# Performance work log

Hardware: AMD Instinct MI355X
Metric: run time of the kernel (lower is better)

## Reference

```python
import jax, jax.numpy as jnp
import numpy as np

NUM_LAYERS = 6
D = 16           # physical_dim == bond_dim (required for multi-layer consistency)
B, S, FIN = 128, 2048, 128


def setup_inputs() -> dict:
    key = jax.random.key(0)
    k0, k1, k2, k3 = jax.random.split(key, 4)
    return {
        "sequence": jax.random.normal(k0, (B, S, FIN), jnp.float32),
        "W_emb": jax.random.normal(k1, (FIN, D), jnp.float32) * 0.05,
        "b_emb": jnp.zeros((D,), jnp.float32),
        "u": jax.random.normal(k2, (NUM_LAYERS, D, D, D, D), jnp.float32) * 0.1,
        "w": jax.random.normal(k3, (NUM_LAYERS, D, D, D), jnp.float32) * 0.1,
    }


def _ent_entropy(sA, sB):
    # sA: (B, pA, d), sB: (B, pB, d)
    corr = jnp.einsum('bik,bjk->bij', sA, sB)          # (B, pA, pB)
    s = jnp.linalg.svd(corr, compute_uv=False)          # (B, min(pA,pB))
    sn = s / (jnp.sum(s, axis=1, keepdims=True) + 1e-8)
    return -jnp.sum(sn * jnp.log(sn + 1e-8), axis=1)    # (B,)


def _phi_q(sites):
    # sites: (B, n, d), n >= 4 and even
    n = sites.shape[1]
    mid = n // 2
    S_int = _ent_entropy(sites[:, :mid], sites[:, mid:])
    A, Bp = sites[:, :mid], sites[:, mid:]
    S1 = _ent_entropy(A[:, :mid // 2], A[:, mid // 2:])
    S2 = _ent_entropy(Bp[:, :(n - mid) // 2], Bp[:, (n - mid) // 2:])
    return jnp.maximum(S_int - (S1 + S2), 0.0)


def _apply_layer(sites, u_l, w_l):
    # sites: (B, n, d) with n even. Disentangle adjacent pairs, then coarse-grain.
    b, n, d = sites.shape
    s = sites.reshape(b, n // 2, 2, d)
    # disentangler: einsum('ijkl,bi,bj->bkl') batched over pairs p
    comb = jnp.einsum('ijkl,bpi,bpj->bpkl', u_l, s[:, :, 0], s[:, :, 1])
    o1 = comb.mean(axis=3)   # mean over l -> (b, p, k)
    o2 = comb.mean(axis=2)   # mean over k -> (b, p, l)
    # isometry acts on consecutive disentangled pairs (o1_i, o2_i)
    return jnp.einsum('aij,bpi,bpj->bpa', w_l, o1, o2)  # (b, n//2, bond)


def reference(sequence, W_emb, b_emb, u, w):
    emb = sequence @ W_emb + b_emb                       # (B, S, D)
    norm = jnp.linalg.norm(emb, axis=-1, keepdims=True)
    sites = emb / jnp.maximum(norm, 1e-12)               # F.normalize(dim=-1)
    for l in range(NUM_LAYERS):
        sites = _apply_layer(sites, u[l], w[l])
    phi_q = _phi_q(sites)
    return sites, phi_q
```

## Files before the change

### kernel.cpp

```cpp
#include <hip/hip_runtime.h>
#include <hip/hip_bf16.h>
#include <math.h>

#define BATCH 128
#define SEQ   2048
#define FIN   128
#define DD    16
#define NLAYERS 6
#define SST   20
#define SWEEPS 8

#define BUFA_F  (BATCH*SEQ*DD)
#define BUFB_F  (BATCH*(SEQ/2)*DD)
#define COEF_OFF (BUFA_F + BUFB_F)
#define ENT_OFF  (COEF_OFF + NLAYERS*12288)

__global__ __launch_bounds__(256) void k_front(const float* __restrict__ seq,
                                               const float* __restrict__ W,
                                               const float* __restrict__ bias,
                                               const float* __restrict__ u,
                                               const float* __restrict__ w,
                                               float* __restrict__ coef,
                                               float* __restrict__ out) {
    __shared__ float sW[2048];
    __shared__ float sR[64*132];
    int t = threadIdx.x;
    if (blockIdx.x < 6) {
        int l  = blockIdx.x;
        int ij = t;
        const float* ub = u + (size_t)l*65536 + (size_t)ij*256;
        float a1[16], a2[16];
#pragma unroll
        for (int k = 0; k < 16; ++k) { a1[k] = 0.0f; a2[k] = 0.0f; }
#pragma unroll
        for (int k = 0; k < 16; ++k) {
#pragma unroll
            for (int z = 0; z < 16; ++z) {
                float v = ub[k*16 + z];
                a1[k] += v;
                a2[z] += v;
            }
        }
        float* ucb = coef + (size_t)l*12288 + ij*32;
#pragma unroll
        for (int k = 0; k < 16; ++k) {
            ucb[k]      = a1[k]*(1.0f/16.0f);
            ucb[16 + k] = a2[k]*(1.0f/16.0f);
        }
        const float* wb = w + (size_t)l*4096;
        float* wtb = coef + (size_t)l*12288 + 8192 + ij*16;
#pragma unroll
        for (int a = 0; a < 16; ++a) wtb[a] = wb[a*256 + ij];
        return;
    }
    size_t rowbase = (size_t)(blockIdx.x - 6) * 64;
    for (int x = t; x < 2048; x += 256) sW[x] = W[x];
    {
        const float4* seq4 = (const float4*)seq + rowbase*32;
#pragma unroll
        for (int it = 0; it < 8; ++it) {
            int idx = t + it*256;
            int r = idx >> 5, kk = idx & 31;
            *(float4*)&sR[r*132 + kk*4] = seq4[idx];
        }
    }
    int q = t & 3, lr = t >> 2;
    float acc[4];
    {
        float4 bv = *(const float4*)(bias + q*4);
        acc[0] = bv.x; acc[1] = bv.y; acc[2] = bv.z; acc[3] = bv.w;
    }
    __syncthreads();

#pragma unroll 8
    for (int kk = 0; kk < 32; ++kk) {
        float4 rv = *(const float4*)&sR[lr*132 + kk*4];
        float rc[4] = { rv.x, rv.y, rv.z, rv.w };
#pragma unroll
        for (int c = 0; c < 4; ++c) {
            float4 wv = *(const float4*)&sW[(kk*4 + c)*16 + q*4];
            float s = rc[c];
            acc[0] = fmaf(s, wv.x, acc[0]);
            acc[1] = fmaf(s, wv.y, acc[1]);
            acc[2] = fmaf(s, wv.z, acc[2]);
            acc[3] = fmaf(s, wv.w, acc[3]);
        }
    }
    float p = 0.0f;
#pragma unroll
    for (int j = 0; j < 4; ++j) p = fmaf(acc[j], acc[j], p);
    p += __shfl_xor(p, 1);
    p += __shfl_xor(p, 2);
    float inv = 1.0f / fmaxf(sqrtf(p), 1e-12f);
    *(float4*)(out + (rowbase + lr)*16 + q*4) = make_float4(acc[0]*inv, acc[1]*inv,
                                                            acc[2]*inv, acc[3]*inv);
}

__global__ __launch_bounds__(256) void k_layer(const float* __restrict__ in,
                                               float* __restrict__ outp,
                                               const float* __restrict__ coefl) {
    __shared__ float cbuf[8192];
    __shared__ float spl[64*36];
    int t = threadIdx.x;
    int og = t & 7, pg = t >> 3;
    int lane = t & 63, base = lane & ~7;

    const float4* wtf = (const float4*)(coefl + 8192);
    float4 wr0 = wtf[0*256 + t];
    float4 wr1 = wtf[1*256 + t];
    float4 wr2 = wtf[2*256 + t];
    float4 wr3 = wtf[3*256 + t];

    {
        const float4* ucf = (const float4*)coefl;
        float4* c4 = (float4*)cbuf;
#pragma unroll
        for (int it = 0; it < 8; ++it) c4[it*256 + t] = ucf[it*256 + t];
    }
    {
        const float4* ing = (const float4*)in + (size_t)blockIdx.x*512;
        float4 v0 = ing[t];
        float4 v1 = ing[t + 256];
        *(float4*)&spl[(t >> 3)*36 + (t & 7)*4]        = v0;
        *(float4*)&spl[((t >> 3) + 32)*36 + (t & 7)*4] = v1;
    }
    __syncthreads();

    float s1v[2][16];
#pragma unroll
    for (int pp = 0; pp < 2; ++pp) {
        int p = pg + pp*32;
#pragma unroll
        for (int g = 0; g < 4; ++g) {
            float4 v = *(const float4*)&spl[p*36 + 16 + g*4];
            s1v[pp][g*4+0]=v.x; s1v[pp][g*4+1]=v.y; s1v[pp][g*4+2]=v.z; s1v[pp][g*4+3]=v.w;
        }
    }

    float accv[2][4];
    accv[0][0]=0.f; accv[0][1]=0.f; accv[0][2]=0.f; accv[0][3]=0.f;
    accv[1][0]=0.f; accv[1][1]=0.f; accv[1][2]=0.f; accv[1][3]=0.f;

    for (int i = 0; i < 16; ++i) {
        float s0a = spl[pg*36 + i];
        float s0b = spl[(pg + 32)*36 + i];
        const float4* uc = (const float4*)&cbuf[i*512] + og;
#pragma unroll
        for (int j = 0; j < 16; ++j) {
            float4 cv = uc[j*8];
            float pa = s0a * s1v[0][j];
            float pb = s0b * s1v[1][j];
            accv[0][0] = fmaf(pa, cv.x, accv[0][0]);
            accv[0][1] = fmaf(pa, cv.y, accv[0][1]);
            accv[0][2] = fmaf(pa, cv.z, accv[0][2]);
            accv[0][3] = fmaf(pa, cv.w, accv[0][3]);
            accv[1][0] = fmaf(pb, cv.x, accv[1][0]);
            accv[1][1] = fmaf(pb, cv.y, accv[1][1]);
            accv[1][2] = fmaf(pb, cv.z, accv[1][2]);
            accv[1][3] = fmaf(pb, cv.w, accv[1][3]);
        }
    }
    __syncthreads();
    {
        float4* c4 = (float4*)cbuf;
        c4[0*256 + t] = wr0;
        c4[1*256 + t] = wr1;
        c4[2*256 + t] = wr2;
        c4[3*256 + t] = wr3;
    }
    __syncthreads();

    float o2f[2][16];
#pragma unroll
    for (int j = 0; j < 16; ++j) {
        int src = base + 4 + (j >> 2);
        o2f[0][j] = __shfl(accv[0][j & 3], src, 64);
        o2f[1][j] = __shfl(accv[1][j & 3], src, 64);
    }

    float r0a = 0.f, r1a = 0.f, r0b = 0.f, r1b = 0.f;
    for (int grp = 0; grp < 4; ++grp) {
#pragma unroll
        for (int c = 0; c < 4; ++c) {
            float o1a = __shfl(accv[0][c], base + grp, 64);
            float o1b = __shfl(accv[1][c], base + grp, 64);
            const float2* wrow = (const float2*)&cbuf[(grp*4 + c)*256] + og;
#pragma unroll
            for (int j = 0; j < 16; ++j) {
                float2 wv = wrow[j*8];
                float qa = o1a * o2f[0][j];
                float qb = o1b * o2f[1][j];
                r0a = fmaf(qa, wv.x, r0a);
                r1a = fmaf(qa, wv.y, r1a);
                r0b = fmaf(qb, wv.x, r0b);
                r1b = fmaf(qb, wv.y, r1b);
            }
        }
    }

    size_t gp = (size_t)blockIdx.x*64;
    *(float2*)&outp[(gp + pg)*16 + og*2]      = make_float2(r0a, r1a);
    *(float2*)&outp[(gp + pg + 32)*16 + og*2] = make_float2(r0b, r1b);
}

template<int P, bool LAST>
__device__ __forceinline__ void layer_body(float* sL, const float* coef,
                                           float* outp, int npg, int t, int bid) {
    int og = t & 7, pg = t >> 3;
    int lane = t & 63, base = lane & ~7;
    bool act = pg < npg;

    float accv[P][4];
    float s1v[P][16];
#pragma unroll
    for (int pp = 0; pp < P; ++pp) { accv[pp][0]=0.f; accv[pp][1]=0.f; accv[pp][2]=0.f; accv[pp][3]=0.f; }

    if (act) {
#pragma unroll
        for (int pp = 0; pp < P; ++pp) {
            int r = 2*(pg + pp*32) + 1;
#pragma unroll
            for (int g = 0; g < 4; ++g) {
                float4 v = *(const float4*)&sL[r*SST + g*4];
                s1v[pp][g*4+0]=v.x; s1v[pp][g*4+1]=v.y; s1v[pp][g*4+2]=v.z; s1v[pp][g*4+3]=v.w;
            }
        }
        for (int i = 0; i < 16; ++i) {
            float s0[P];
#pragma unroll
            for (int pp = 0; pp < P; ++pp) s0[pp] = sL[(2*(pg + pp*32))*SST + i];
            const float4* uc = (const float4*)&coef[i*512] + og;
#pragma unroll
            for (int j = 0; j < 16; ++j) {
                float4 cv = uc[j*8];
#pragma unroll
                for (int pp = 0; pp < P; ++pp) {
                    float p = s0[pp] * s1v[pp][j];
                    accv[pp][0] = fmaf(p, cv.x, accv[pp][0]);
                    accv[pp][1] = fmaf(p, cv.y, accv[pp][1]);
                    accv[pp][2] = fmaf(p, cv.z, accv[pp][2]);
                    accv[pp][3] = fmaf(p, cv.w, accv[pp][3]);
                }
            }
        }
    }
    __syncthreads();

    if (act) {
        float o2f[P][16];
#pragma unroll
        for (int j = 0; j < 16; ++j) {
            int src = base + 4 + (j >> 2);
#pragma unroll
            for (int pp = 0; pp < P; ++pp)
                o2f[pp][j] = __shfl(accv[pp][j & 3], src, 64);
        }
        float r0[P], r1[P];
#pragma unroll
        for (int pp = 0; pp < P; ++pp) { r0[pp] = 0.f; r1[pp] = 0.f; }
        for (int grp = 0; grp < 4; ++grp) {
#pragma unroll
            for (int c = 0; c < 4; ++c) {
                float o1i[P];
#pragma unroll
                for (int pp = 0; pp < P; ++pp)
                    o1i[pp] = __shfl(accv[pp][c], base + grp, 64);
#pragma unroll
                for (int j = 0; j < 16; ++j) {
                    float2 wv = *(const float2*)&coef[8192 + ((grp*4+c)*16 + j)*16 + og*2];
#pragma unroll
                    for (int pp = 0; pp < P; ++pp) {
                        float q = o1i[pp] * o2f[pp][j];
                        r0[pp] = fmaf(q, wv.x, r0[pp]);
                        r1[pp] = fmaf(q, wv.y, r1[pp]);
                    }
                }
            }
        }
        if (LAST) {
#pragma unroll
            for (int pp = 0; pp < P; ++pp) {
                int p = pg + pp*32;
                *(float2*)&outp[((size_t)bid*32 + p)*16 + og*2] = make_float2(r0[pp], r1[pp]);
            }
        } else {
#pragma unroll
            for (int pp = 0; pp < P; ++pp) {
                int p = pg + pp*32;
                *(float2*)&sL[p*SST + og*2] = make_float2(r0[pp], r1[pp]);
            }
        }
    }
    __syncthreads();
}

__global__ __launch_bounds__(256) void k_tail(const float* __restrict__ in,
                                              const float* __restrict__ coefg,
                                              float* __restrict__ outp) {
    __shared__ float coef[12288];
    __shared__ float sL[256*SST];
    int t = threadIdx.x, bid = blockIdx.x;

    const float4* in4 = (const float4*)in + (size_t)bid*1024;
#pragma unroll
    for (int it = 0; it < 4; ++it) {
        int f = it*256 + t;
        *(float4*)&sL[(f >> 2)*SST + (f & 3)*4] = in4[f];
    }
#pragma unroll 1
    for (int l = 0; l < 3; ++l) {
        const float4* src = (const float4*)(coefg + (size_t)(3 + l)*12288);
        __syncthreads();
        for (int x = t; x < 3072; x += 256) ((float4*)coef)[x] = src[x];
        __syncthreads();
        switch (l) {
            case 0: layer_body<4,false>(sL, coef, outp, 32, t, bid); break;
            case 1: layer_body<2,false>(sL, coef, outp, 32, t, bid); break;
            case 2: layer_body<1,true >(sL, coef, outp, 32, t, bid); break;
        }
    }
}

__device__ __forceinline__ void rot_cs(float al, float be, float ga, float& c, float& s) {
    float ze = (be - al) / (2.0f * ga);
    float tt = copysignf(1.0f, ze) / (fabsf(ze) + sqrtf(1.0f + ze*ze));
    c = 1.0f / sqrtf(1.0f + tt*tt);
    s = c * tt;
}

__global__ __launch_bounds__(64) void k_phi(const float* __restrict__ sites,
                                            float* __restrict__ ent) {
    __shared__ float S[512];
    __shared__ float C[256];
    __shared__ float sv[16];
    int bid = blockIdx.x;
    int role = bid >> 7;
    int b = bid & 127;
    int t = threadIdx.x;
    const float* sp = sites + (size_t)b*512;

    if (role == 0) {
        for (int x = t; x < 512; x += 64) S[x] = sp[x];
        __syncthreads();
        for (int e = t; e < 256; e += 64) {
            int i = e & 15, j = e >> 4;
            float a = 0.0f;
            for (int k = 0; k < 16; ++k) a = fmaf(S[i*16+k], S[(16+j)*16+k], a);
            C[j*16 + i] = a;
        }
        __syncthreads();
        for (int sw = 0; sw < SWEEPS; ++sw) {
            for (int r = 0; r < 15; ++r) {
                int pr = t >> 3, sub = t & 7;
                int p, q;
                if (pr == 0) { p = 15; q = r; }
                else { p = (r + pr) % 15; q = (r + 15 - pr) % 15; }
                float u0 = C[p*16 + 2*sub],   u1v = C[p*16 + 2*sub + 1];
                float v0 = C[q*16 + 2*sub],   v1v = C[q*16 + 2*sub + 1];
                float al = u0*u0 + u1v*u1v;
                float be = v0*v0 + v1v*v1v;
                float ga = u0*v0 + u1v*v1v;
                al += __shfl_xor(al,1); al += __shfl_xor(al,2); al += __shfl_xor(al,4);
                be += __shfl_xor(be,1); be += __shfl_xor(be,2); be += __shfl_xor(be,4);
                ga += __shfl_xor(ga,1); ga += __shfl_xor(ga,2); ga += __shfl_xor(ga,4);
                if (ga != 0.0f) {
                    float c, s; rot_cs(al, be, ga, c, s);
                    C[p*16 + 2*sub]     = fmaf(c, u0, -s*v0);
                    C[p*16 + 2*sub + 1] = fmaf(c, u1v, -s*v1v);
                    C[q*16 + 2*sub]     = fmaf(s, u0,  c*v0);
                    C[q*16 + 2*sub + 1] = fmaf(s, u1v, c*v1v);
                }
                __syncthreads();
            }
        }
        if (t < 16) {
            float s2 = 0.0f;
            for (int rr = 0; rr < 16; ++rr) { float v = C[t*16+rr]; s2 = fmaf(v, v, s2); }
            sv[t] = sqrtf(s2);
        }
        __syncthreads();
        if (t == 0) {
            float sum = 0.0f;
            for (int i2 = 0; i2 < 16; ++i2) sum += sv[i2];
            float den = sum + 1e-8f;
            float e2 = 0.0f;
            for (int i2 = 0; i2 < 16; ++i2) {
                float sn = sv[i2] / den;
                e2 -= sn * logf(sn + 1e-8f);
            }
            ent[b] = e2;
        }
    } else {
        int ro = (role == 1) ? 0 : 256;
        for (int x = t; x < 256; x += 64) S[x] = sp[ro + x];
        __syncthreads();
        if (t < 64) {
            int i = t & 7, j = t >> 3;
            float a = 0.0f;
            for (int k = 0; k < 16; ++k) a = fmaf(S[i*16+k], S[(8+j)*16+k], a);
            C[j*8 + i] = a;
        }
        __syncthreads();
        for (int sw = 0; sw < SWEEPS; ++sw) {
            for (int r = 0; r < 7; ++r) {
                if (t < 32) {
                    int pr = t >> 3, sub = t & 7;
                    int p, q;
                    if (pr == 0) { p = 7; q = r; }
                    else { p = (r + pr) % 7; q = (r + 7 - pr) % 7; }
                    float uu = C[p*8 + sub], vv = C[q*8 + sub];
                    float al = uu*uu, be = vv*vv, ga = uu*vv;
                    al += __shfl_xor(al,1); al += __shfl_xor(al,2); al += __shfl_xor(al,4);
                    be += __shfl_xor(be,1); be += __shfl_xor(be,2); be += __shfl_xor(be,4);
                    ga += __shfl_xor(ga,1); ga += __shfl_xor(ga,2); ga += __shfl_xor(ga,4);
                    if (ga != 0.0f) {
                        float c, s; rot_cs(al, be, ga, c, s);
                        C[p*8 + sub] = fmaf(c, uu, -s*vv);
                        C[q*8 + sub] = fmaf(s, uu,  c*vv);
                    }
                }
                __syncthreads();
            }
        }
        if (t < 8) {
            float s2 = 0.0f;
            for (int rr = 0; rr < 8; ++rr) { float v = C[t*8+rr]; s2 = fmaf(v, v, s2); }
            sv[t] = sqrtf(s2);
        }
        __syncthreads();
        if (t == 0) {
            float sum = 0.0f;
            for (int i2 = 0; i2 < 8; ++i2) sum += sv[i2];
            float den = sum + 1e-8f;
            float e2 = 0.0f;
            for (int i2 = 0; i2 < 8; ++i2) {
                float sn = sv[i2] / den;
                e2 -= sn * logf(sn + 1e-8f);
            }
            ent[role*128 + b] = e2;
        }
    }
}

__global__ __launch_bounds__(128) void k_phi2(const float* __restrict__ ent,
                                              float* __restrict__ phi) {
    int b = threadIdx.x;
    phi[b] = fmaxf(ent[b] - (ent[128 + b] + ent[256 + b]), 0.0f);
}

extern "C" void kernel_launch(void* const* d_in, const int* in_sizes, int n_in,
                              void* d_out, int out_size, void* d_ws, size_t ws_size,
                              hipStream_t stream) {
    const float* seq  = (const float*)d_in[0];
    const float* W    = (const float*)d_in[1];
    const float* bias = (const float*)d_in[2];
    const float* u    = (const float*)d_in[3];
    const float* w    = (const float*)d_in[4];
    float* out = (float*)d_out;
    float* ws  = (float*)d_ws;

    float* bufA  = ws;
    float* bufB  = ws + BUFA_F;
    float* coefw = ws + COEF_OFF;
    float* entb  = ws + ENT_OFF;

    k_front<<<6 + (BATCH*SEQ)/64, 256, 0, stream>>>(seq, W, bias, u, w, coefw, bufA);

    k_layer<<<2048, 256, 0, stream>>>(bufA, bufB, coefw + 0*12288);
    k_layer<<<1024, 256, 0, stream>>>(bufB, bufA, coefw + 1*12288);
    k_layer<<< 512, 256, 0, stream>>>(bufA, bufB, coefw + 2*12288);
    k_tail <<< 128, 256, 0, stream>>>(bufB, coefw, out);

    k_phi <<<3*BATCH, 64, 0, stream>>>(out, entb);
    k_phi2<<<1, 128, 0, stream>>>(entb, out + BATCH*32*DD);
}
```

Before: 211.5 us.

## Fuse embedding projection with first MERA layer in one kernel

Coefficient preparation moves into its own small kernel, and the embedding GEMM plus normalization is fused with the first disentangler/isometry layer. Each block embeds 128 rows into shared memory and applies layer 0 directly. This removes the global write and read of the full normalized embedding buffer (128x2048x16 floats) and one launch. In exchange it adds a separate prep launch that must finish before the fused kernel, and higher shared-memory use per block.

```diff
diff --git a/kernel.cpp b/kernel.cpp
--- a/kernel.cpp
+++ b/kernel.cpp
@@ -15,85 +15,185 @@
 #define COEF_OFF (BUFA_F + BUFB_F)
 #define ENT_OFF  (COEF_OFF + NLAYERS*12288)
 
-__global__ __launch_bounds__(256) void k_front(const float* __restrict__ seq,
+__global__ __launch_bounds__(256) void k_prep(const float* __restrict__ u,
+                                              const float* __restrict__ w,
+                                              float* __restrict__ coef) {
+    int l  = blockIdx.x;
+    int ij = threadIdx.x;
+    const float* ub = u + (size_t)l*65536 + (size_t)ij*256;
+    float a1[16], a2[16];
+#pragma unroll
+    for (int k = 0; k < 16; ++k) { a1[k] = 0.0f; a2[k] = 0.0f; }
+#pragma unroll
+    for (int k = 0; k < 16; ++k) {
+#pragma unroll
+        for (int z = 0; z < 16; ++z) {
+            float v = ub[k*16 + z];
+            a1[k] += v;
+            a2[z] += v;
+        }
+    }
+    float* ucb = coef + (size_t)l*12288 + ij*32;
+#pragma unroll
+    for (int k = 0; k < 16; ++k) {
+        ucb[k]      = a1[k]*(1.0f/16.0f);
+        ucb[16 + k] = a2[k]*(1.0f/16.0f);
+    }
+    const float* wb = w + (size_t)l*4096;
+    float* wtb = coef + (size_t)l*12288 + 8192 + ij*16;
+#pragma unroll
+    for (int a = 0; a < 16; ++a) wtb[a] = wb[a*256 + ij];
+}
+
+__global__ __launch_bounds__(256) void k_mega1(const float* __restrict__ seq,
                                                const float* __restrict__ W,
                                                const float* __restrict__ bias,
-                                               const float* __restrict__ u,
-                                               const float* __restrict__ w,
-                                               float* __restrict__ coef,
-                                               float* __restrict__ out) {
-    __shared__ float sW[2048];
-    __shared__ float sR[64*132];
+                                               const float* __restrict__ coef0,
+                                               float* __restrict__ outp) {
+    __shared__ float pool[13056];
+    float* sW   = pool;
+    float* sR   = pool + 2048;
+    float* cbuf = pool + 2048;
+    float* sL   = pool + 10496;
     int t = threadIdx.x;
-    if (blockIdx.x < 6) {
-        int l  = blockIdx.x;
-        int ij = t;
-        const float* ub = u + (size_t)l*65536 + (size_t)ij*256;
-        float a1[16], a2[16];
-#pragma unroll
-        for (int k = 0; k < 16; ++k) { a1[k] = 0.0f; a2[k] = 0.0f; }
-#pragma unroll
-        for (int k = 0; k < 16; ++k) {
-#pragma unroll
-            for (int z = 0; z < 16; ++z) {
-                float v = ub[k*16 + z];
-                a1[k] += v;
-                a2[z] += v;
-            }
-        }
-        float* ucb = coef + (size_t)l*12288 + ij*32;
-#pragma unroll
-        for (int k = 0; k < 16; ++k) {
-            ucb[k]      = a1[k]*(1.0f/16.0f);
-            ucb[16 + k] = a2[k]*(1.0f/16.0f);
-        }
-        const float* wb = w + (size_t)l*4096;
-        float* wtb = coef + (size_t)l*12288 + 8192 + ij*16;
-#pragma unroll
-        for (int a = 0; a < 16; ++a) wtb[a] = wb[a*256 + ij];
-        return;
-    }
-    size_t rowbase = (size_t)(blockIdx.x - 6) * 64;
-    for (int x = t; x < 2048; x += 256) sW[x] = W[x];
+    int og = t & 7, pg = t >> 3;
+    int lane = t & 63, base = lane & ~7;
+
+    const float4* wtf = (const float4*)(coef0 + 8192);
+    float4 wr0 = wtf[0*256 + t];
+    float4 wr1 = wtf[1*256 + t];
+    float4 wr2 = wtf[2*256 + t];
+    float4 wr3 = wtf[3*256 + t];
+
     {
-        const float4* seq4 = (const float4*)seq + rowbase*32;
-#pragma unroll
-        for (int it = 0; it < 8; ++it) {
-            int idx = t + it*256;
-            int r = idx >> 5, kk = idx & 31;
-            *(float4*)&sR[r*132 + kk*4] = seq4[idx];
-        }
-    }
+        const float4* W4 = (const float4*)W;
+        ((float4*)sW)[t]       = W4[t];
+        ((float4*)sW)[t + 256] = W4[t + 256];
+    }
+
     int q = t & 3, lr = t >> 2;
-    float acc[4];
+    float4 bv = *(const float4*)(bias + q*4);
+    size_t rowbase = (size_t)blockIdx.x * 128;
+
+#pragma unroll 1
+    for (int ps = 0; ps < 2; ++ps) {
+        {
+            const float4* seq4 = (const float4*)seq + (rowbase + ps*64)*32;
+#pragma unroll
+            for (int it = 0; it < 8; ++it) {
+                int idx = it*256 + t;
+                *(float4*)&sR[(idx >> 5)*132 + (idx & 31)*4] = seq4[idx];
+            }
+        }
+        __syncthreads();
+        float acc[4] = { bv.x, bv.y, bv.z, bv.w };
+#pragma unroll 8
+        for (int kk = 0; kk < 32; ++kk) {
+            float4 rv = *(const float4*)&sR[lr*132 + kk*4];
+            float rc[4] = { rv.x, rv.y, rv.z, rv.w };
+#pragma unroll
+            for (int c = 0; c < 4; ++c) {
+                float4 wv = *(const float4*)&sW[(kk*4 + c)*16 + q*4];
+                float s = rc[c];
+                acc[0] = fmaf(s, wv.x, acc[0]);
+                acc[1] = fmaf(s, wv.y, acc[1]);
+                acc[2] = fmaf(s, wv.z, acc[2]);
+                acc[3] = fmaf(s, wv.w, acc[3]);
+            }
+        }
+        float p = 0.0f;
+#pragma unroll
+        for (int j = 0; j < 4; ++j) p = fmaf(acc[j], acc[j], p);
+        p += __shfl_xor(p, 1);
+        p += __shfl_xor(p, 2);
+        float inv = 1.0f / fmaxf(sqrtf(p), 1e-12f);
+        *(float4*)&sL[(ps*64 + lr)*SST + q*4] = make_float4(acc[0]*inv, acc[1]*inv,
+                                                            acc[2]*inv, acc[3]*inv);
+        __syncthreads();
+    }
+
     {
-        float4 bv = *(const float4*)(bias + q*4);
-        acc[0] = bv.x; acc[1] = bv.y; acc[2] = bv.z; acc[3] = bv.w;
-    }
-    __syncthreads();
-
-#pragma unroll 8
-    for (int kk = 0; kk < 32; ++kk) {
-        float4 rv = *(const float4*)&sR[lr*132 + kk*4];
-        float rc[4] = { rv.x, rv.y, rv.z, rv.w };
+        const float4* ucf = (const float4*)coef0;
+        float4* c4 = (float4*)cbuf;
+#pragma unroll
+        for (int it = 0; it < 8; ++it) c4[it*256 + t] = ucf[it*256 + t];
+    }
+    __syncthreads();
+
+    float s1v[2][16];
+#pragma unroll
+    for (int pp = 0; pp < 2; ++pp) {
+        int p = pg + pp*32;
+#pragma unroll
+        for (int g = 0; g < 4; ++g) {
+            float4 v = *(const float4*)&sL[(2*p + 1)*SST + g*4];
+            s1v[pp][g*4+0]=v.x; s1v[pp][g*4+1]=v.y; s1v[pp][g*4+2]=v.z; s1v[pp][g*4+3]=v.w;
+        }
+    }
+    float accv[2][4];
+    accv[0][0]=0.f; accv[0][1]=0.f; accv[0][2]=0.f; accv[0][3]=0.f;
+    accv[1][0]=0.f; accv[1][1]=0.f; accv[1][2]=0.f; accv[1][3]=0.f;
+
+    for (int i = 0; i < 16; ++i) {
+        float s0a = sL[(2*pg)*SST + i];
+        float s0b = sL[(2*(pg + 32))*SST + i];
+        const float4* uc = (const float4*)&cbuf[i*512] + og;
+#pragma unroll
+        for (int j = 0; j < 16; ++j) {
+            float4 cv = uc[j*8];
+            float pa = s0a * s1v[0][j];
+            float pb = s0b * s1v[1][j];
+            accv[0][0] = fmaf(pa, cv.x, accv[0][0]);
+            accv[0][1] = fmaf(pa, cv.y, accv[0][1]);
+            accv[0][2] = fmaf(pa, cv.z, accv[0][2]);
+            accv[0][3] = fmaf(pa, cv.w, accv[0][3]);
+            accv[1][0] = fmaf(pb, cv.x, accv[1][0]);
+            accv[1][1] = fmaf(pb, cv.y, accv[1][1]);
+            accv[1][2] = fmaf(pb, cv.z, accv[1][2]);
+            accv[1][3] = fmaf(pb, cv.w, accv[1][3]);
+        }
+    }
+    __syncthreads();
+    {
+        float4* c4 = (float4*)cbuf;
+        c4[0*256 + t] = wr0;
+        c4[1*256 + t] = wr1;
+        c4[2*256 + t] = wr2;
+        c4[3*256 + t] = wr3;
+    }
+    __syncthreads();
+
+    float o2f[2][16];
+#pragma unroll
+    for (int j = 0; j < 16; ++j) {
+        int src = base + 4 + (j >> 2);
+        o2f[0][j] = __shfl(accv[0][j & 3], src, 64);
+        o2f[1][j] = __shfl(accv[1][j & 3], src, 64);
+    }
+
+    float r0a = 0.f, r1a = 0.f, r0b = 0.f, r1b = 0.f;
+    for (int grp = 0; grp < 4; ++grp) {
 #pragma unroll
         for (int c = 0; c < 4; ++c) {
-            float4 wv = *(const float4*)&sW[(kk*4 + c)*16 + q*4];
-            float s = rc[c];
-            acc[0] = fmaf(s, wv.x, acc[0]);
-            acc[1] = fmaf(s, wv.y, acc[1]);
-            acc[2] = fmaf(s, wv.z, acc[2]);
-            acc[3] = fmaf(s, wv.w, acc[3]);
-        }
-    }
-    float p = 0.0f;
-#pragma unroll
-    for (int j = 0; j < 4; ++j) p = fmaf(acc[j], acc[j], p);
-    p += __shfl_xor(p, 1);
-    p += __shfl_xor(p, 2);
-    float inv = 1.0f / fmaxf(sqrtf(p), 1e-12f);
-    *(float4*)(out + (rowbase + lr)*16 + q*4) = make_float4(acc[0]*inv, acc[1]*inv,
-                                                            acc[2]*inv, acc[3]*inv);
+            float o1a = __shfl(accv[0][c], base + grp, 64);
+            float o1b = __shfl(accv[1][c], base + grp, 64);
+            const float2* wrow = (const float2*)&cbuf[(grp*4 + c)*256] + og;
+#pragma unroll
+            for (int j = 0; j < 16; ++j) {
+                float2 wv = wrow[j*8];
+                float qa = o1a * o2f[0][j];
+                float qb = o1b * o2f[1][j];
+                r0a = fmaf(qa, wv.x, r0a);
+                r1a = fmaf(qa, wv.y, r1a);
+                r0b = fmaf(qb, wv.x, r0b);
+                r1b = fmaf(qb, wv.y, r1b);
+            }
+        }
+    }
+
+    size_t gp = (size_t)blockIdx.x*64;
+    *(float2*)&outp[(gp + pg)*16 + og*2]      = make_float2(r0a, r1a);
+    *(float2*)&outp[(gp + pg + 32)*16 + og*2] = make_float2(r0b, r1b);
 }
 
 __global__ __launch_bounds__(256) void k_layer(const float* __restrict__ in,
@@ -464,9 +564,10 @@
     float* coefw = ws + COEF_OFF;
     float* entb  = ws + ENT_OFF;
 
-    k_front<<<6 + (BATCH*SEQ)/64, 256, 0, stream>>>(seq, W, bias, u, w, coefw, bufA);
-
-    k_layer<<<2048, 256, 0, stream>>>(bufA, bufB, coefw + 0*12288);
+    k_prep <<<NLAYERS, 256, 0, stream>>>(u, w, coefw);
+
+    k_mega1<<<(BATCH*SEQ)/128, 256, 0, stream>>>(seq, W, bias, coefw, bufB);
+
     k_layer<<<1024, 256, 0, stream>>>(bufB, bufA, coefw + 1*12288);
     k_layer<<< 512, 256, 0, stream>>>(bufA, bufB, coefw + 2*12288);
     k_tail <<< 128, 256, 0, stream>>>(bufB, coefw, out);
```

Measured after the change: 225.5 us. 1.07x slower.
